# Optimization experiments

Measured on AMD Instinct MI355X. Metric: run time of the kernel, lower is better.

Reference implementation:

```python
import jax, jax.numpy as jnp
import numpy as np

THETA = 10000.0
NUM_HEADS = 16


def _rope(x, positions):
    # x: [B, H, S, Dk] (fp32), positions: [B, S] int
    d_k = x.shape[-1]
    k = jnp.arange(0, d_k, 2, dtype=jnp.float32)
    freqs = THETA ** (-k / d_k)                      # [Dk/2]
    angles = positions[..., None].astype(jnp.float32) * freqs  # [B, S, Dk/2]
    cos = jnp.cos(angles)[:, None, :, :]             # [B, 1, S, Dk/2]
    sin = jnp.sin(angles)[:, None, :, :]
    xr = x.reshape(*x.shape[:-1], d_k // 2, 2)
    x_even, x_odd = xr[..., 0], xr[..., 1]
    rot_even = x_even * cos - x_odd * sin
    rot_odd = x_even * sin + x_odd * cos
    out = jnp.stack([rot_even, rot_odd], axis=-1)
    return out.reshape(x.shape)


def setup_inputs() -> dict:
    key = jax.random.key(0)
    ks = jax.random.split(key, 6)
    B, S, D = 2, 2048, 1024
    std = (2.0 / (D + D)) ** 0.5
    x = jax.random.normal(ks[0], (B, S, D), dtype=jnp.float32)
    Wq = jax.random.normal(ks[1], (D, D), dtype=jnp.float32) * std
    Wk = jax.random.normal(ks[2], (D, D), dtype=jnp.float32) * std
    Wv = jax.random.normal(ks[3], (D, D), dtype=jnp.float32) * std
    Wo = jax.random.normal(ks[4], (D, D), dtype=jnp.float32) * std
    token_positions = jnp.broadcast_to(jnp.arange(S, dtype=jnp.int32), (B, S))
    return {"x": x, "Wq": Wq, "Wk": Wk, "Wv": Wv, "Wo": Wo,
            "token_positions": token_positions}


def reference(x, Wq, Wk, Wv, Wo, token_positions):
    B, S, D = x.shape
    H = NUM_HEADS
    Dk = D // H
    # QKV projections (no bias): y = x @ W.T
    def proj(W):
        return (x @ W.T).reshape(B, S, H, Dk).transpose(0, 2, 1, 3)  # [B,H,S,Dk]
    Q, K, V = proj(Wq), proj(Wk), proj(Wv)
    Q = _rope(Q, token_positions)
    K = _rope(K, token_positions)
    scale = 1.0 / jnp.sqrt(jnp.float32(Dk))
    scores = jnp.einsum('bhqd,bhkd->bhqk', Q, K) * scale  # [B,H,S,S]
    causal = jnp.tril(jnp.ones((S, S), dtype=bool))
    scores = jnp.where(causal, scores, -jnp.inf)
    attn = jax.nn.softmax(scores.astype(jnp.float32), axis=-1)
    out = jnp.einsum('bhqk,bhkd->bhqd', attn, V)          # [B,H,S,Dk]
    out = out.transpose(0, 2, 1, 3).reshape(B, S, D)
    return out @ Wo.T
```

## Files before the change

### kernel.cpp

```cpp
#include <hip/hip_runtime.h>
#include <math.h>

#define D_MODEL 1024
#define NHEADS 16
#define DK 64
#define SEQ 2048
#define BATCH 2
#define MROWS (BATCH * SEQ)

typedef __attribute__((ext_vector_type(8))) short bfrag8;
typedef __attribute__((ext_vector_type(4))) float f32x4;
typedef unsigned short u16;
typedef __attribute__((ext_vector_type(8))) u16 u16x8;
typedef __attribute__((ext_vector_type(4))) u16 u16x4;

#define GLOBAL_AS(p) ((const __attribute__((address_space(1))) void*)(p))
#define LDS_AS(p)    ((__attribute__((address_space(3))) void*)(p))

#define RAW_BARRIER()  __asm__ volatile("s_barrier" ::: "memory")
#define WAIT_VM2()     __asm__ volatile("s_waitcnt vmcnt(2)" ::: "memory")
#define WAIT_VM0()     __asm__ volatile("s_waitcnt vmcnt(0)" ::: "memory")

__device__ inline u16 f2bf(float f) {
  union { float f; unsigned u; } c; c.f = f;
  unsigned r = c.u + 0x7FFF + ((c.u >> 16) & 1);
  return (u16)(r >> 16);
}

__device__ inline unsigned pack_bf2(float lo, float hi) {
  return __builtin_amdgcn_perm(__float_as_uint(hi), __float_as_uint(lo), 0x07060302);
}

struct CvtPtrs { const float* src[5]; };

__global__ __launch_bounds__(256)
void convert_and_tab(CvtPtrs p, u16* __restrict__ dst,
                     const int* __restrict__ pos, float2* __restrict__ tab) {
  const int bi = blockIdx.x;
  if (bi < 8192) {
    size_t base = ((size_t)bi * 256 + threadIdx.x) * 4;
    const size_t XSZ = (size_t)MROWS * D_MODEL;
    const float* s; size_t off;
    if (base < XSZ) { s = p.src[0]; off = base; }
    else {
      size_t j = base - XSZ;
      s = p.src[1 + (int)(j >> 20)];
      off = j & ((1u << 20) - 1);
    }
    float4 v = *(const float4*)(s + off);
    u16 o[4] = { f2bf(v.x), f2bf(v.y), f2bf(v.z), f2bf(v.w) };
    *(u16x4*)(dst + base) = *(u16x4*)o;
  } else {
    int idx = (bi - 8192) * 256 + threadIdx.x;
    int i = idx & 31, bs = idx >> 5;
    float pp = (float)pos[bs];
    float freq = expf(-(float)i * 0.2878231366242558f);
    float sn, cs;
    sincosf(pp * freq, &sn, &cs);
    tab[idx] = make_float2(cs, sn);
  }
}

__device__ inline void gemm_core(const u16* __restrict__ A, const u16* __restrict__ B,
                                 int m0, int n0, u16* As, u16* Bs,
                                 f32x4 acc[4][4]) {
  const int tid = threadIdx.x;
  const int w = tid >> 6, lane = tid & 63;
  const int l15 = lane & 15, quad = lane >> 4;
  const int wm = w >> 1, wn = w & 1;
  const int srow = tid >> 2;
  const int scol = (tid & 3) * 8;

  #pragma unroll
  for (int mi = 0; mi < 4; ++mi)
    #pragma unroll
    for (int ni = 0; ni < 4; ++ni) acc[mi][ni] = (f32x4)0.f;

  for (int k0 = 0; k0 < D_MODEL; k0 += 32) {
    __syncthreads();
    #pragma unroll
    for (int i = 0; i < 2; ++i) {
      const u16* ga = A + (size_t)((i * 64 + srow) + m0) * D_MODEL + k0 + scol;
      const u16* gb = B + (size_t)((i * 64 + srow) + n0) * D_MODEL + k0 + scol;
      __builtin_amdgcn_global_load_lds(GLOBAL_AS(ga), LDS_AS(&As[(i * 64 + w * 16) * 32]), 16, 0, 0);
      __builtin_amdgcn_global_load_lds(GLOBAL_AS(gb), LDS_AS(&Bs[(i * 64 + w * 16) * 32]), 16, 0, 0);
    }
    __syncthreads();

    bfrag8 af[4], bfr[4];
    #pragma unroll
    for (int i = 0; i < 4; ++i) {
      af[i]  = *(const bfrag8*)&As[(wm * 64 + i * 16 + l15) * 32 + quad * 8];
      bfr[i] = *(const bfrag8*)&Bs[(wn * 64 + i * 16 + l15) * 32 + quad * 8];
    }
    #pragma unroll
    for (int mi = 0; mi < 4; ++mi)
      #pragma unroll
      for (int ni = 0; ni < 4; ++ni)
        acc[mi][ni] = __builtin_amdgcn_mfma_f32_16x16x32_bf16(af[mi], bfr[ni], acc[mi][ni], 0, 0, 0);
  }
}

struct QKVArgs { const u16* A[3]; const u16* B[3]; u16* dst[3]; const float2* tab; };

__global__ __launch_bounds__(256)
void gemm_qkv_fused(QKVArgs p) {
  __shared__ u16 As[128 * 32];
  __shared__ u16 Bs[128 * 32];
  const int z = blockIdx.z;
  const int bi = blockIdx.x;
  int m0, n0;
  if (z < 2) { m0 = (bi & 7) * 128; n0 = (bi >> 3) * 128; }
  else       { m0 = (bi >> 3) * 128; n0 = (bi & 7) * 128; }
  f32x4 acc[4][4];
  gemm_core(p.A[z], p.B[z], m0, n0, As, Bs, acc);

  const int tid = threadIdx.x;
  const int w = tid >> 6, lane = tid & 63;
  const int l15 = lane & 15, quad = lane >> 4;
  const int wm = w >> 1, wn = w & 1;
  u16* dst = p.dst[z];

  if (z < 2) {
    const int head = (m0 + wm * 64) >> 6;
    const float scale = (z == 0) ? 0.125f * 1.4426950408889634f : 1.0f;
    #pragma unroll
    for (int ni = 0; ni < 4; ++ni) {
      int sg = n0 + wn * 64 + ni * 16 + l15;
      int b = sg >> 11;
      int s = sg & (SEQ - 1);
      size_t ho = ((size_t)(b * NHEADS + head)) * SEQ * DK;
      #pragma unroll
      for (int mi = 0; mi < 4; ++mi) {
        float4 t = *(const float4*)&p.tab[(size_t)sg * 32 + mi * 8 + quad * 2];
        float e0 = acc[mi][ni][0], o0 = acc[mi][ni][1];
        float e1 = acc[mi][ni][2], o1 = acc[mi][ni][3];
        u16x4 ov = { f2bf((e0 * t.x - o0 * t.y) * scale),
                     f2bf((e0 * t.y + o0 * t.x) * scale),
                     f2bf((e1 * t.z - o1 * t.w) * scale),
                     f2bf((e1 * t.w + o1 * t.z) * scale) };
        *(u16x4*)&dst[ho + (size_t)s * DK + mi * 16 + quad * 4] = ov;
      }
    }
  } else {
    const int b = m0 >> 11;
    const int head = (n0 >> 6) + wn;
    const size_t ho = ((size_t)(b * NHEADS + head)) * SEQ * DK;
    const int row_base = m0 + wm * 64;
    #pragma unroll
    for (int mi = 0; mi < 4; ++mi)
      #pragma unroll
      for (int ni = 0; ni < 4; ++ni) {
        int d = ni * 16 + l15;
        int sb = (row_base + mi * 16 + quad * 4) & (SEQ - 1);
        u16 o[4];
        #pragma unroll
        for (int r = 0; r < 4; ++r) o[r] = f2bf(acc[mi][ni][r]);
        *(u16x4*)&dst[ho + (size_t)d * SEQ + sb] = *(u16x4*)o;
      }
  }
}

__global__ __launch_bounds__(256)
void gemm_out_bf16(const u16* __restrict__ A, const u16* __restrict__ B,
                   float* __restrict__ C) {
  __shared__ u16 As[128 * 32];
  __shared__ u16 Bs[64 * 32];
  const int m0 = blockIdx.y * 128, n0 = blockIdx.x * 64;
  const int tid = threadIdx.x;
  const int w = tid >> 6, lane = tid & 63;
  const int l15 = lane & 15, quad = lane >> 4;
  const int wm = w >> 1, wn = w & 1;
  const int lrow = lane >> 2;
  const int lcol = (lane & 3) * 8;

  f32x4 acc[4][2];
  #pragma unroll
  for (int mi = 0; mi < 4; ++mi)
    #pragma unroll
    for (int ni = 0; ni < 2; ++ni) acc[mi][ni] = (f32x4)0.f;

  for (int k0 = 0; k0 < D_MODEL; k0 += 32) {
    __syncthreads();
    #pragma unroll
    for (int i = 0; i < 2; ++i) {
      int row = (i * 4 + w) * 16 + lrow;
      const u16* ga = A + (size_t)(m0 + row) * D_MODEL + k0 + lcol;
      __builtin_amdgcn_global_load_lds(GLOBAL_AS(ga), LDS_AS(&As[(i * 4 + w) * 16 * 32]), 16, 0, 0);
    }
    {
      int row = w * 16 + lrow;
      const u16* gb = B + (size_t)(n0 + row) * D_MODEL + k0 + lcol;
      __builtin_amdgcn_global_load_lds(GLOBAL_AS(gb), LDS_AS(&Bs[w * 16 * 32]), 16, 0, 0);
    }
    __syncthreads();

    bfrag8 af[4], bfr[2];
    #pragma unroll
    for (int i = 0; i < 4; ++i)
      af[i] = *(const bfrag8*)&As[(wm * 64 + i * 16 + l15) * 32 + quad * 8];
    #pragma unroll
    for (int i = 0; i < 2; ++i)
      bfr[i] = *(const bfrag8*)&Bs[(wn * 32 + i * 16 + l15) * 32 + quad * 8];
    #pragma unroll
    for (int mi = 0; mi < 4; ++mi)
      #pragma unroll
      for (int ni = 0; ni < 2; ++ni)
        acc[mi][ni] = __builtin_amdgcn_mfma_f32_16x16x32_bf16(af[mi], bfr[ni], acc[mi][ni], 0, 0, 0);
  }

  #pragma unroll
  for (int mi = 0; mi < 4; ++mi)
    #pragma unroll
    for (int ni = 0; ni < 2; ++ni)
      #pragma unroll
      for (int r = 0; r < 4; ++r) {
        int row = m0 + wm * 64 + mi * 16 + quad * 4 + r;
        int col = n0 + wn * 32 + ni * 16 + l15;
        C[(size_t)row * D_MODEL + col] = acc[mi][ni][r];
      }
}

#define PSTR 72

__global__ __launch_bounds__(512)
void attn_mfma(const u16* __restrict__ Qbf, const u16* __restrict__ Kbf,
               const u16* __restrict__ Vtb, u16* __restrict__ obb) {
  __shared__ u16 Ks[2][64 * 64];
  __shared__ u16 Vt[2][64 * 64];
  __shared__ u16 Ps[8][16 * PSTR];

  const int tid = threadIdx.x;
  const int w = tid >> 6, lane = tid & 63;
  const int l15 = lane & 15, quad = lane >> 4;
  const int hb = blockIdx.x >> 4;
  const int qp = blockIdx.x & 15;
  const int qt = (w < 4) ? qp : (31 - qp);
  const int b = hb >> 4, h = hb & 15;
  const size_t ho = (size_t)hb * SEQ * DK;
  const int qrow_base = qt * 64 + (w & 3) * 16;

  bfrag8 qf[2];
  #pragma unroll
  for (int hh = 0; hh < 2; ++hh)
    qf[hh] = *(const bfrag8*)&Qbf[ho + (size_t)(qrow_base + l15) * DK + hh * 32 + quad * 8];

  f32x4 oacc[4];
  float l_ = 0.f;
  #pragma unroll
  for (int n0 = 0; n0 < 4; ++n0) oacc[n0] = (f32x4)0.f;

  const int srow = w * 8 + (lane >> 3);
  const int scc = ((lane & 7) ^ (srow & 7)) * 8;

  #define STAGE(T, BUF) do {                                                         \
    int j0_ = (T) * 64;                                                              \
    __builtin_amdgcn_global_load_lds(GLOBAL_AS(Kbf + ho + (size_t)(j0_ + srow) * DK + scc), \
                                     LDS_AS(&Ks[BUF][w * 512]), 16, 0, 0);           \
    __builtin_amdgcn_global_load_lds(GLOBAL_AS(Vtb + ho + (size_t)srow * SEQ + j0_ + scc), \
                                     LDS_AS(&Vt[BUF][w * 512]), 16, 0, 0);           \
  } while (0)

  const int ntiles = 32 - qp;
  STAGE(0, 0);

  for (int t = 0; t < ntiles; ++t) {
    const int j0 = t * 64;
    const int buf = t & 1;
    RAW_BARRIER();
    if (t + 1 < ntiles) {
      STAGE(t + 1, buf ^ 1);
      WAIT_VM2();
    } else {
      WAIT_VM0();
    }
    RAW_BARRIER();

    if (t > qt) continue;

    f32x4 sc[4];
    const int sw = l15 & 7;
    #pragma unroll
    for (int st = 0; st < 4; ++st) {
      int key = st * 16 + l15;
      bfrag8 kf0 = *(const bfrag8*)&Ks[buf][key * 64 + ((quad ^ sw) * 8)];
      bfrag8 kf1 = *(const bfrag8*)&Ks[buf][key * 64 + (((4 + quad) ^ sw) * 8)];
      sc[st] = __builtin_amdgcn_mfma_f32_16x16x32_bf16(kf0, qf[0], (f32x4)0.f, 0, 0, 0);
      sc[st] = __builtin_amdgcn_mfma_f32_16x16x32_bf16(kf1, qf[1], sc[st], 0, 0, 0);
    }

    if (j0 + 63 > qrow_base) {
      #pragma unroll
      for (int st = 0; st < 4; ++st)
        #pragma unroll
        for (int r = 0; r < 4; ++r) {
          int key = j0 + st * 16 + quad * 4 + r;
          if (key > qrow_base + l15) sc[st][r] = -60.f;
        }
    }

    float pv[4][4], rs = 0.f;
    #pragma unroll
    for (int st = 0; st < 4; ++st)
      #pragma unroll
      for (int r = 0; r < 4; ++r) {
        pv[st][r] = __builtin_amdgcn_exp2f(fminf(sc[st][r], 60.f));
        rs += pv[st][r];
      }
    l_ += rs;

    #pragma unroll
    for (int st = 0; st < 4; ++st) {
      uint2 pk = { pack_bf2(pv[st][0], pv[st][1]), pack_bf2(pv[st][2], pv[st][3]) };
      *(uint2*)&Ps[w][l15 * PSTR + st * 16 + quad * 4] = pk;
    }
    __asm__ volatile("s_waitcnt lgkmcnt(0)" ::: "memory");

    bfrag8 pf[2];
    #pragma unroll
    for (int kc = 0; kc < 2; ++kc)
      pf[kc] = *(const bfrag8*)&Ps[w][l15 * PSTR + kc * 32 + quad * 8];
    #pragma unroll
    for (int n0 = 0; n0 < 4; ++n0) {
      #pragma unroll
      for (int kc = 0; kc < 2; ++kc) {
        bfrag8 vf = *(const bfrag8*)&Vt[buf][(n0 * 16 + l15) * 64 + (((kc * 4 + quad) ^ sw) * 8)];
        oacc[n0] = __builtin_amdgcn_mfma_f32_16x16x32_bf16(vf, pf[kc], oacc[n0], 0, 0, 0);
      }
    }
  }
  #undef STAGE

  float l = l_;
  l += __shfl_xor(l, 16);
  l += __shfl_xor(l, 32);
  float inv = 1.f / l;
  int q = qrow_base + l15;
  #pragma unroll
  for (int n0 = 0; n0 < 4; ++n0) {
    u16x4 ov = { f2bf(oacc[n0][0] * inv), f2bf(oacc[n0][1] * inv),
                 f2bf(oacc[n0][2] * inv), f2bf(oacc[n0][3] * inv) };
    *(u16x4*)&obb[(size_t)(b * SEQ + q) * D_MODEL + h * DK + n0 * 16 + quad * 4] = ov;
  }
}

extern "C" void kernel_launch(void* const* d_in, const int* in_sizes, int n_in,
                              void* d_out, int out_size, void* d_ws, size_t ws_size,
                              hipStream_t stream) {
  const float* x  = (const float*)d_in[0];
  const float* Wq = (const float*)d_in[1];
  const float* Wk = (const float*)d_in[2];
  const float* Wv = (const float*)d_in[3];
  const float* Wo = (const float*)d_in[4];
  const int* pos  = (const int*)d_in[5];

  const size_t XSZ = (size_t)MROWS * D_MODEL;
  const size_t WSZ = (size_t)D_MODEL * D_MODEL;

  u16* bfb = (u16*)d_ws;
  u16* xb  = bfb;
  u16* wqb = xb  + XSZ;
  u16* wkb = wqb + WSZ;
  u16* wvb = wkb + WSZ;
  u16* wob = wvb + WSZ;
  u16* Qbf = wob + WSZ;
  u16* Kbf = Qbf + XSZ;
  u16* Vtb = Kbf + XSZ;
  u16* obb = Vtb + XSZ;
  float2* tab = (float2*)(obb + XSZ);

  CvtPtrs cp; cp.src[0] = x; cp.src[1] = Wq; cp.src[2] = Wk; cp.src[3] = Wv; cp.src[4] = Wo;
  convert_and_tab<<<8192 + 512, 256, 0, stream>>>(cp, xb, pos, tab);

  QKVArgs qp;
  qp.A[0] = wqb; qp.A[1] = wkb; qp.A[2] = xb;
  qp.B[0] = xb;  qp.B[1] = xb;  qp.B[2] = wvb;
  qp.dst[0] = Qbf; qp.dst[1] = Kbf; qp.dst[2] = Vtb;
  qp.tab = tab;
  gemm_qkv_fused<<<dim3(256, 1, 3), 256, 0, stream>>>(qp);

  attn_mfma<<<dim3(512), 512, 0, stream>>>(Qbf, Kbf, Vtb, obb);

  gemm_out_bf16<<<dim3(D_MODEL / 64, MROWS / 128), 256, 0, stream>>>(obb, wob, (float*)d_out);
}
```

Baseline: 188.5 us.

## Split attention blocks per query tile and swap LDS P-staging for ds_bpermute

Attention blocks shrink from 512 to 256 threads, each covering a single 64-row query tile instead of a paired light/heavy tile. The grid doubles and block IDs are mapped so light and heavy tiles interleave, which removes idle waves on skipped tiles. Each K/V stage load is now issued by fewer waves, and the bf16 probability fragments are transposed with ds_bpermute cross-lane shuffles rather than a round trip through shared memory. This cuts LDS usage and a wait on lgkmcnt, but adds bpermute traffic and relies on per-block scheduling to balance the causal load.

```diff
diff --git a/kernel.cpp b/kernel.cpp
--- a/kernel.cpp
+++ b/kernel.cpp
@@ -18,7 +18,7 @@
 #define LDS_AS(p)    ((__attribute__((address_space(3))) void*)(p))
 
 #define RAW_BARRIER()  __asm__ volatile("s_barrier" ::: "memory")
-#define WAIT_VM2()     __asm__ volatile("s_waitcnt vmcnt(2)" ::: "memory")
+#define WAIT_VM4()     __asm__ volatile("s_waitcnt vmcnt(4)" ::: "memory")
 #define WAIT_VM0()     __asm__ volatile("s_waitcnt vmcnt(0)" ::: "memory")
 
 __device__ inline u16 f2bf(float f) {
@@ -221,24 +221,24 @@
       }
 }
 
-#define PSTR 72
-
-__global__ __launch_bounds__(512)
+__global__ __launch_bounds__(256, 4)
 void attn_mfma(const u16* __restrict__ Qbf, const u16* __restrict__ Kbf,
                const u16* __restrict__ Vtb, u16* __restrict__ obb) {
   __shared__ u16 Ks[2][64 * 64];
   __shared__ u16 Vt[2][64 * 64];
-  __shared__ u16 Ps[8][16 * PSTR];
 
   const int tid = threadIdx.x;
   const int w = tid >> 6, lane = tid & 63;
   const int l15 = lane & 15, quad = lane >> 4;
-  const int hb = blockIdx.x >> 4;
-  const int qp = blockIdx.x & 15;
-  const int qt = (w < 4) ? qp : (31 - qp);
+
+  const int bid = blockIdx.x;
+  const int hb = bid & 31;
+  const int g  = bid >> 5;
+  const int tt = (g & 7) | ((g & 16) >> 1);
+  const int qt = (g & 8) ? (31 - tt) : tt;
   const int b = hb >> 4, h = hb & 15;
   const size_t ho = (size_t)hb * SEQ * DK;
-  const int qrow_base = qt * 64 + (w & 3) * 16;
+  const int qrow_base = qt * 64 + w * 16;
 
   bfrag8 qf[2];
   #pragma unroll
@@ -253,15 +253,22 @@
   const int srow = w * 8 + (lane >> 3);
   const int scc = ((lane & 7) ^ (srow & 7)) * 8;
 
+  const int adr0 = (((quad & 1) << 5) + l15) << 2;
+  const int adr1 = adr0 + 64;
+
   #define STAGE(T, BUF) do {                                                         \
     int j0_ = (T) * 64;                                                              \
-    __builtin_amdgcn_global_load_lds(GLOBAL_AS(Kbf + ho + (size_t)(j0_ + srow) * DK + scc), \
-                                     LDS_AS(&Ks[BUF][w * 512]), 16, 0, 0);           \
-    __builtin_amdgcn_global_load_lds(GLOBAL_AS(Vtb + ho + (size_t)srow * SEQ + j0_ + scc), \
-                                     LDS_AS(&Vt[BUF][w * 512]), 16, 0, 0);           \
+    _Pragma("unroll")                                                                \
+    for (int r_ = 0; r_ < 2; ++r_) {                                                 \
+      int row_ = r_ * 32 + srow;                                                     \
+      __builtin_amdgcn_global_load_lds(GLOBAL_AS(Kbf + ho + (size_t)(j0_ + row_) * DK + scc), \
+                                       LDS_AS(&Ks[BUF][(r_ * 32 + w * 8) * 64]), 16, 0, 0);   \
+      __builtin_amdgcn_global_load_lds(GLOBAL_AS(Vtb + ho + (size_t)row_ * SEQ + j0_ + scc),  \
+                                       LDS_AS(&Vt[BUF][(r_ * 32 + w * 8) * 64]), 16, 0, 0);   \
+    }                                                                                \
   } while (0)
 
-  const int ntiles = 32 - qp;
+  const int ntiles = qt + 1;
   STAGE(0, 0);
 
   for (int t = 0; t < ntiles; ++t) {
@@ -270,13 +277,11 @@
     RAW_BARRIER();
     if (t + 1 < ntiles) {
       STAGE(t + 1, buf ^ 1);
-      WAIT_VM2();
+      WAIT_VM4();
     } else {
       WAIT_VM0();
     }
     RAW_BARRIER();
-
-    if (t > qt) continue;
 
     f32x4 sc[4];
     const int sw = l15 & 7;
@@ -299,27 +304,33 @@
         }
     }
 
-    float pv[4][4], rs = 0.f;
-    #pragma unroll
-    for (int st = 0; st < 4; ++st)
-      #pragma unroll
-      for (int r = 0; r < 4; ++r) {
-        pv[st][r] = __builtin_amdgcn_exp2f(fminf(sc[st][r], 60.f));
-        rs += pv[st][r];
-      }
+    unsigned pk[4][2];
+    float rs = 0.f;
+    #pragma unroll
+    for (int st = 0; st < 4; ++st) {
+      float p0 = __builtin_amdgcn_exp2f(fminf(sc[st][0], 60.f));
+      float p1 = __builtin_amdgcn_exp2f(fminf(sc[st][1], 60.f));
+      float p2 = __builtin_amdgcn_exp2f(fminf(sc[st][2], 60.f));
+      float p3 = __builtin_amdgcn_exp2f(fminf(sc[st][3], 60.f));
+      rs += (p0 + p1) + (p2 + p3);
+      pk[st][0] = pack_bf2(p0, p1);
+      pk[st][1] = pack_bf2(p2, p3);
+    }
     l_ += rs;
 
-    #pragma unroll
-    for (int st = 0; st < 4; ++st) {
-      uint2 pk = { pack_bf2(pv[st][0], pv[st][1]), pack_bf2(pv[st][2], pv[st][3]) };
-      *(uint2*)&Ps[w][l15 * PSTR + st * 16 + quad * 4] = pk;
-    }
-    __asm__ volatile("s_waitcnt lgkmcnt(0)" ::: "memory");
-
-    bfrag8 pf[2];
-    #pragma unroll
-    for (int kc = 0; kc < 2; ++kc)
-      pf[kc] = *(const bfrag8*)&Ps[w][l15 * PSTR + kc * 32 + quad * 8];
+    union PU { bfrag8 f; int i[4]; } u0, u1;
+    #pragma unroll
+    for (int j = 0; j < 4; ++j) {
+      const int adr = (j & 2) ? adr1 : adr0;
+      int lo0 = __builtin_amdgcn_ds_bpermute(adr, (int)pk[0][j & 1]);
+      int hi0 = __builtin_amdgcn_ds_bpermute(adr, (int)pk[1][j & 1]);
+      int lo1 = __builtin_amdgcn_ds_bpermute(adr, (int)pk[2][j & 1]);
+      int hi1 = __builtin_amdgcn_ds_bpermute(adr, (int)pk[3][j & 1]);
+      u0.i[j] = (quad & 2) ? hi0 : lo0;
+      u1.i[j] = (quad & 2) ? hi1 : lo1;
+    }
+    bfrag8 pf[2] = { u0.f, u1.f };
+
     #pragma unroll
     for (int n0 = 0; n0 < 4; ++n0) {
       #pragma unroll
@@ -379,7 +390,7 @@
   qp.tab = tab;
   gemm_qkv_fused<<<dim3(256, 1, 3), 256, 0, stream>>>(qp);
 
-  attn_mfma<<<dim3(512), 512, 0, stream>>>(Qbf, Kbf, Vtb, obb);
+  attn_mfma<<<dim3(1024), 256, 0, stream>>>(Qbf, Kbf, Vtb, obb);
 
   gemm_out_bf16<<<dim3(D_MODEL / 64, MROWS / 128), 256, 0, stream>>>(obb, wob, (float*)d_out);
 }
```

Measured after the change: 182.7 us. -3.1%, faster.
